# Kernel tuning notes

Hardware: AMD Instinct MI355X
Metric: run time of the kernel (lower is better)

## Reference

```python
import jax, jax.numpy as jnp
import numpy as np

HIDDEN = 768
HEADS = 12
HEAD_DIM = HIDDEN // HEADS

def setup_inputs() -> dict:
    key = jax.random.key(0)
    ks = jax.random.split(key, 9)
    s = 1.0 / np.sqrt(HIDDEN)
    x = jax.random.normal(ks[0], (2, 2048, HIDDEN), dtype=jnp.float32)
    Wq = jax.random.normal(ks[1], (HIDDEN, HIDDEN), dtype=jnp.float32) * s
    bq = jnp.zeros((HIDDEN,), dtype=jnp.float32)
    Wk = jax.random.normal(ks[2], (HIDDEN, HIDDEN), dtype=jnp.float32) * s
    bk = jnp.zeros((HIDDEN,), dtype=jnp.float32)
    Wv = jax.random.normal(ks[3], (HIDDEN, HIDDEN), dtype=jnp.float32) * s
    bv = jnp.zeros((HIDDEN,), dtype=jnp.float32)
    Wo = jax.random.normal(ks[4], (HIDDEN, HIDDEN), dtype=jnp.float32) * s
    bo = jnp.zeros((HIDDEN,), dtype=jnp.float32)
    return {"x": x, "Wq": Wq, "bq": bq, "Wk": Wk, "bk": bk,
            "Wv": Wv, "bv": bv, "Wo": Wo, "bo": bo}

def reference(x, Wq, bq, Wk, bk, Wv, bv, Wo, bo):
    B, S, _ = x.shape
    # project and split heads: [B, H, S, D]
    def proj(W, b):
        return (x @ W + b).reshape(B, S, HEADS, HEAD_DIM).transpose(0, 2, 1, 3)
    q = proj(Wq, bq)
    k = proj(Wk, bk)
    v = proj(Wv, bv)
    # NOTE: original module does NOT scale by 1/sqrt(head_dim)
    scores = jnp.einsum('bhqd,bhkd->bhqk', q, k)
    attn = jax.nn.softmax(scores, axis=-1)
    out = jnp.einsum('bhqk,bhkd->bhqd', attn, v)
    out = out.transpose(0, 2, 1, 3).reshape(B, S, HIDDEN)
    return out @ Wo + bo
```

## Files before the change

### kernel.cpp

```cpp
#include <hip/hip_runtime.h>
#include <cstddef>

#define HIDDEN 768
#define NHEADS 12
#define HDIM   64
#define BATCH  2
#define SEQ    2048
#define NROWS  (BATCH*SEQ)
#define LOG2E  1.4426950408889634f

typedef float f32x4  __attribute__((ext_vector_type(4)));
typedef float f32x16 __attribute__((ext_vector_type(16)));
typedef short bf16x8 __attribute__((ext_vector_type(8)));

__device__ __forceinline__ float fast_exp2(float x){
    return __builtin_amdgcn_exp2f(x);
}

__device__ __forceinline__ unsigned short f2bf(float f){
    unsigned u = __builtin_bit_cast(unsigned, f);
    u = u + 0x7FFFu + ((u >> 16) & 1u);
    return (unsigned short)(u >> 16);
}
__device__ __forceinline__ unsigned packbf2(float a, float b){
    unsigned ua = (__builtin_bit_cast(unsigned, a) + 0x8000u) >> 16;
    unsigned ub = (__builtin_bit_cast(unsigned, b) + 0x8000u) & 0xFFFF0000u;
    return ua | ub;
}
__device__ __forceinline__ unsigned cvtpk_bf16(float a, float b){
    unsigned r;
    asm("v_cvt_pk_bf16_f32 %0, %1, %2" : "=v"(r) : "v"(a), "v"(b));
    return r;
}

__device__ __forceinline__ void gl_lds16(const unsigned short* g, unsigned short* l){
    __builtin_amdgcn_global_load_lds(
        (const __attribute__((address_space(1))) unsigned int*)g,
        (__attribute__((address_space(3))) unsigned int*)l, 16, 0, 0);
}

__global__ __launch_bounds__(256) void cvt_bf16(const float* __restrict__ in,
                                                unsigned short* __restrict__ out,
                                                int n4)
{
    const int i = blockIdx.x * 256 + threadIdx.x;
    if (i >= n4) return;
    const float4 v = reinterpret_cast<const float4*>(in)[i];
    ushort4 o;
    o.x = f2bf(v.x); o.y = f2bf(v.y); o.z = f2bf(v.z); o.w = f2bf(v.w);
    reinterpret_cast<ushort4*>(out)[i] = o;
}

__global__ __launch_bounds__(256) void transpose_cvt4(const float* __restrict__ W0,
                                                      const float* __restrict__ W1,
                                                      const float* __restrict__ W2,
                                                      const float* __restrict__ W3,
                                                      unsigned short* __restrict__ T0,
                                                      unsigned short* __restrict__ T1,
                                                      unsigned short* __restrict__ T2,
                                                      unsigned short* __restrict__ T3)
{
    const int z = blockIdx.z;
    const float* W = (z == 0) ? W0 : (z == 1) ? W1 : (z == 2) ? W2 : W3;
    unsigned short* Wt = (z == 0) ? T0 : (z == 1) ? T1 : (z == 2) ? T2 : T3;

    __shared__ unsigned short t[64][66];
    const int k0 = blockIdx.y * 64, n0 = blockIdx.x * 64;
    const int row = threadIdx.x >> 2;
    const int c0  = (threadIdx.x & 3) * 16;
#pragma unroll
    for (int j = 0; j < 16; j += 4) {
        const float4 v = *reinterpret_cast<const float4*>(&W[(size_t)(k0 + row) * HIDDEN + n0 + c0 + j]);
        t[row][c0 + j + 0] = f2bf(v.x);
        t[row][c0 + j + 1] = f2bf(v.y);
        t[row][c0 + j + 2] = f2bf(v.z);
        t[row][c0 + j + 3] = f2bf(v.w);
    }
    __syncthreads();
#pragma unroll
    for (int j = 0; j < 16; j += 4) {
        ushort4 o;
        o.x = t[c0 + j + 0][row];
        o.y = t[c0 + j + 1][row];
        o.z = t[c0 + j + 2][row];
        o.w = t[c0 + j + 3][row];
        *reinterpret_cast<ushort4*>(&Wt[(size_t)(n0 + row) * HIDDEN + k0 + c0 + j]) = o;
    }
}

__device__ __forceinline__ void gemm_body(const unsigned short* __restrict__ A,
                                          const unsigned short* __restrict__ Wt,
                                          const float* __restrict__ bias,
                                          void* __restrict__ Cout, int mode,
                                          float scale,
                                          unsigned short* As, unsigned short* Bs)
{
    const int tid = threadIdx.x;
    const int l = tid & 63, w = tid >> 6;
    const int wm = w >> 1, wn = w & 1;
    const int l15 = l & 15, lg = l >> 4;
    const int srow = l >> 3, sslot = l & 7;
    const int m0 = blockIdx.y * 64, n0 = blockIdx.x * 96;

    f32x4 acc[2][3] = {};

    for (int k0 = 0; k0 < HIDDEN; k0 += 64) {
        __syncthreads();
#pragma unroll
        for (int a = 0; a < 2; ++a) {
            const int row = (a * 4 + w) * 8 + srow;
            const int sl = sslot ^ (row & 7);
            gl_lds16(&A[(size_t)(m0 + row) * HIDDEN + k0 + sl * 8], &As[(a * 4 + w) * 512]);
        }
#pragma unroll
        for (int b = 0; b < 3; ++b) {
            const int row = (b * 4 + w) * 8 + srow;
            const int sl = sslot ^ (row & 7);
            gl_lds16(&Wt[(size_t)(n0 + row) * HIDDEN + k0 + sl * 8], &Bs[(b * 4 + w) * 512]);
        }
        __syncthreads();

#pragma unroll
        for (int kk = 0; kk < 2; ++kk) {
            bf16x8 af[2], bfr[3];
#pragma unroll
            for (int mi = 0; mi < 2; ++mi) {
                const int r = wm * 32 + mi * 16 + l15;
                af[mi] = *reinterpret_cast<const bf16x8*>(&As[r * 64 + ((lg * 8 + kk * 32) ^ ((r & 7) << 3))]);
            }
#pragma unroll
            for (int ni = 0; ni < 3; ++ni) {
                const int r = wn * 48 + ni * 16 + l15;
                bfr[ni] = *reinterpret_cast<const bf16x8*>(&Bs[r * 64 + ((lg * 8 + kk * 32) ^ ((r & 7) << 3))]);
            }
#pragma unroll
            for (int mi = 0; mi < 2; ++mi)
#pragma unroll
                for (int ni = 0; ni < 3; ++ni)
                    acc[mi][ni] = __builtin_amdgcn_mfma_f32_16x16x32_bf16(af[mi], bfr[ni], acc[mi][ni], 0, 0, 0);
        }
    }

#pragma unroll
    for (int mi = 0; mi < 2; ++mi) {
#pragma unroll
        for (int ni = 0; ni < 3; ++ni) {
#pragma unroll
            for (int rr = 0; rr < 4; ++rr) {
                const int row = m0 + wm * 32 + mi * 16 + lg * 4 + rr;
                const int col = n0 + wn * 48 + ni * 16 + l15;
                const float v = (acc[mi][ni][rr] + bias[col]) * scale;
                if (mode == 0) {
                    const int b = row >> 11, s = row & (SEQ - 1);
                    const int hh = col >> 6, d = col & (HDIM - 1);
                    ((unsigned short*)Cout)[(((size_t)b * NHEADS + hh) * SEQ + s) * HDIM + d] = f2bf(v);
                } else if (mode == 1) {
                    const int b = row >> 11, s = row & (SEQ - 1);
                    const int hh = col >> 6, d = col & (HDIM - 1);
                    ((unsigned short*)Cout)[(((size_t)b * NHEADS + hh) * HDIM + d) * SEQ + s] = f2bf(v);
                } else {
                    ((float*)Cout)[(size_t)row * HIDDEN + col] = v;
                }
            }
        }
    }
}

__global__ __launch_bounds__(256) void qkv_gemm(const unsigned short* __restrict__ A,
                                                const unsigned short* __restrict__ Wqt,
                                                const unsigned short* __restrict__ Wkt,
                                                const unsigned short* __restrict__ Wvt,
                                                const float* __restrict__ bq,
                                                const float* __restrict__ bk,
                                                const float* __restrict__ bv,
                                                unsigned short* __restrict__ Qb,
                                                unsigned short* __restrict__ Kb,
                                                unsigned short* __restrict__ Vtb)
{
    __shared__ unsigned short As[64 * 64];
    __shared__ unsigned short Bs[96 * 64];
    const int z = blockIdx.z;
    const unsigned short* Wt = (z == 0) ? Wqt : (z == 1) ? Wkt : Wvt;
    const float* bias = (z == 0) ? bq : (z == 1) ? bk : bv;
    void* out = (z == 0) ? (void*)Qb : (z == 1) ? (void*)Kb : (void*)Vtb;
    const int mode = (z == 2) ? 1 : 0;
    const float scale = (z == 0) ? LOG2E : 1.0f;
    gemm_body(A, Wt, bias, out, mode, scale, As, Bs);
}

__global__ __launch_bounds__(256) void out_gemm(const unsigned short* __restrict__ A,
                                                const unsigned short* __restrict__ Wt,
                                                const float* __restrict__ bias,
                                                float* __restrict__ Cout)
{
    __shared__ unsigned short As[64 * 64];
    __shared__ unsigned short Bs[96 * 64];
    gemm_body(A, Wt, bias, Cout, 2, 1.0f, As, Bs);
}

__global__ __launch_bounds__(256, 4) void attn_mfma(const unsigned short* __restrict__ Q,
                                                    const unsigned short* __restrict__ K,
                                                    const unsigned short* __restrict__ Vt,
                                                    unsigned short* __restrict__ O)
{
    __shared__ __align__(16) char shraw[32768];
    unsigned short* shus = (unsigned short*)shraw;
    float*          pub  = (float*)shraw;
    float2*         mlx  = (float2*)(shraw + 24576);
    unsigned int*   Ep   = (unsigned int*)shraw;

    const int tid = threadIdx.x;
    const int l = tid & 63, w = tid >> 6;
    const int l31 = l & 31, hi = l >> 5;
    const int q0 = blockIdx.x * 32;
    const int h = blockIdx.y, b = blockIdx.z;
    const size_t base = ((size_t)b * NHEADS + h) * (size_t)SEQ * HDIM;

    unsigned short* Kb = shus + w * 4096;
    unsigned short* Vb = Kb + 2048;

    const int q = q0 + l31;
    bf16x8 qf[4];
#pragma unroll
    for (int t = 0; t < 4; ++t)
        qf[t] = *reinterpret_cast<const bf16x8*>(&Q[base + (size_t)q * HDIM + 16 * t + 8 * hi]);

    f32x16 accO[2] = {};
    float m = -1e30f, lsum = 0.f;

    const int klr = l >> 3, kslot = l & 7;
    const int vdl = l & 15, vjs = l >> 4;

    for (int t = 0; t < 16; ++t) {
        const int t0 = w * (SEQ / 4) + t * 32;

        asm volatile("s_waitcnt lgkmcnt(0)" ::: "memory");
#pragma unroll
        for (int c = 0; c < 4; ++c) {
            const int row = c * 8 + klr;
            const int sl = kslot ^ (row & 7);
            gl_lds16(&K[base + (size_t)(t0 + row) * HDIM + sl * 8], &Kb[c * 512]);
        }
#pragma unroll
        for (int c = 0; c < 4; ++c) {
            gl_lds16(&Vt[base + (size_t)(c * 16 + vdl) * SEQ + t0 + vjs * 8], &Vb[c * 512]);
        }
        asm volatile("s_waitcnt vmcnt(0)" ::: "memory");
        __builtin_amdgcn_sched_barrier(0);

        f32x16 sv = {};
        __builtin_amdgcn_s_setprio(1);
#pragma unroll
        for (int tt = 0; tt < 4; ++tt) {
            const int co = 16 * tt + 8 * hi;
            const bf16x8 kf = *reinterpret_cast<const bf16x8*>(&Kb[l31 * 64 + (co ^ ((l31 & 7) << 3))]);
            sv = __builtin_amdgcn_mfma_f32_32x32x16_bf16(kf, qf[tt], sv, 0, 0, 0);
        }
        __builtin_amdgcn_s_setprio(0);

        float tmax = -1e30f;
#pragma unroll
        for (int r = 0; r < 16; r += 4)
            tmax = fmaxf(tmax, fmaxf(fmaxf(sv[r], sv[r + 1]), fmaxf(sv[r + 2], sv[r + 3])));
        tmax = fmaxf(tmax, __shfl_xor(tmax, 32));

        if (tmax > m + 8.f) {
            const float scl = fast_exp2(m - tmax);
            lsum *= scl;
#pragma unroll
            for (int r = 0; r < 16; ++r) { accO[0][r] *= scl; accO[1][r] *= scl; }
            m = tmax;
        }

        unsigned wv[8];
        float ls = 0.f;
#pragma unroll
        for (int a = 0; a < 8; ++a) {
            const float pa = fast_exp2(sv[2 * a] - m);
            const float pb = fast_exp2(sv[2 * a + 1] - m);
            ls += pa + pb;
            wv[a] = cvtpk_bf16(pa, pb);
        }
        ls += __shfl_xor(ls, 32);
        lsum += ls;

#pragma unroll
        for (int s2 = 0; s2 < 2; ++s2) {
            const unsigned w0 = wv[s2 * 4 + 0], w1 = wv[s2 * 4 + 1];
            const unsigned w2 = wv[s2 * 4 + 2], w3 = wv[s2 * 4 + 3];
            const unsigned x0 = (unsigned)__shfl_xor((int)w0, 32);
            const unsigned x1 = (unsigned)__shfl_xor((int)w1, 32);
            const unsigned x2 = (unsigned)__shfl_xor((int)w2, 32);
            const unsigned x3 = (unsigned)__shfl_xor((int)w3, 32);
            uint4 fr;
            fr.x = hi ? x2 : w0;
            fr.y = hi ? x3 : w1;
            fr.z = hi ? w2 : x0;
            fr.w = hi ? w3 : x1;
            const bf16x8 pfrag = __builtin_bit_cast(bf16x8, fr);
            __builtin_amdgcn_s_setprio(1);
#pragma unroll
            for (int db = 0; db < 2; ++db) {
                const int d = 32 * db + l31;
                const int js = 2 * s2 + hi;
                const bf16x8 vf = *reinterpret_cast<const bf16x8*>(
                    &Vb[(d >> 4) * 512 + (js * 16 + (d & 15)) * 8]);
                accO[db] = __builtin_amdgcn_mfma_f32_32x32x16_bf16(vf, pfrag, accO[db], 0, 0, 0);
            }
            __builtin_amdgcn_s_setprio(0);
        }
    }

    __syncthreads();
    if (!hi) mlx[w * 32 + l31] = make_float2(m, lsum);
    __syncthreads();
    float M = -1e30f;
    float mj[4], lj[4];
#pragma unroll
    for (int j = 0; j < 4; ++j) {
        const float2 tml = mlx[j * 32 + l31];
        mj[j] = tml.x; lj[j] = tml.y;
        M = fmaxf(M, tml.x);
    }
    float lf = 0.f;
#pragma unroll
    for (int j = 0; j < 4; ++j) lf += lj[j] * fast_exp2(mj[j] - M);
    const float s = fast_exp2(m - M);
    const float inv = 1.f / lf;

    if (w != 0) {
#pragma unroll
        for (int db = 0; db < 2; ++db)
#pragma unroll
            for (int r = 0; r < 16; ++r) {
                const int d = 32 * db + (r & 3) + 8 * (r >> 2) + 4 * hi;
                pub[(w - 1) * 2048 + l31 * 64 + ((d + l31) & 63)] = accO[db][r] * s;
            }
    }
    __syncthreads();
    if (w == 0) {
#pragma unroll
        for (int db = 0; db < 2; ++db)
#pragma unroll
            for (int r = 0; r < 16; ++r) {
                const int d = 32 * db + (r & 3) + 8 * (r >> 2) + 4 * hi;
                float v = accO[db][r] * s;
#pragma unroll
                for (int wi = 0; wi < 3; ++wi)
                    v += pub[wi * 2048 + l31 * 64 + ((d + l31) & 63)];
                accO[db][r] = v * inv;
            }
        asm volatile("s_waitcnt lgkmcnt(0)" ::: "memory");
        __builtin_amdgcn_sched_barrier(0);
#pragma unroll
        for (int db = 0; db < 2; ++db)
#pragma unroll
            for (int a = 0; a < 8; ++a) {
                const unsigned wd = packbf2(accO[db][2 * a], accO[db][2 * a + 1]);
                const int pi = 16 * db + 4 * (a >> 1) + (a & 1) + 2 * hi;
                Ep[l31 * 33 + pi] = wd;
            }
        asm volatile("s_waitcnt lgkmcnt(0)" ::: "memory");
        __builtin_amdgcn_sched_barrier(0);
#pragma unroll
        for (int pss = 0; pss < 4; ++pss) {
            const int idx = pss * 64 + l;
            const int qr = idx >> 3, c = idx & 7;
            uint4 ov;
            ov.x = Ep[qr * 33 + c * 4 + 0];
            ov.y = Ep[qr * 33 + c * 4 + 1];
            ov.z = Ep[qr * 33 + c * 4 + 2];
            ov.w = Ep[qr * 33 + c * 4 + 3];
            *reinterpret_cast<uint4*>(&O[((size_t)b * SEQ + q0 + qr) * HIDDEN + h * HDIM + c * 8]) = ov;
        }
    }
}

extern "C" void kernel_launch(void* const* d_in, const int* in_sizes, int n_in,
                              void* d_out, int out_size, void* d_ws, size_t ws_size,
                              hipStream_t stream)
{
    const float* x  = (const float*)d_in[0];
    const float* Wq = (const float*)d_in[1];
    const float* bq = (const float*)d_in[2];
    const float* Wk = (const float*)d_in[3];
    const float* bk = (const float*)d_in[4];
    const float* Wv = (const float*)d_in[5];
    const float* bv = (const float*)d_in[6];
    const float* Wo = (const float*)d_in[7];
    const float* bo = (const float*)d_in[8];
    float* out = (float*)d_out;

    unsigned short* p = (unsigned short*)d_ws;
    const size_t szX = (size_t)NROWS * HIDDEN;
    const size_t szW = (size_t)HIDDEN * HIDDEN;
    const size_t szH = (size_t)BATCH * NHEADS * SEQ * HDIM;
    unsigned short* xb  = p;              p += szX;
    unsigned short* Wqt = p;              p += szW;
    unsigned short* Wkt = p;              p += szW;
    unsigned short* Wvt = p;              p += szW;
    unsigned short* Wot = p;              p += szW;
    unsigned short* Qb  = p;              p += szH;
    unsigned short* Kb  = p;              p += szH;
    unsigned short* Vtb = p;              p += szH;
    unsigned short* Oab = p;              p += szX;

    cvt_bf16<<<(int)(szX / 4 + 255) / 256, 256, 0, stream>>>(x, xb, (int)(szX / 4));
    transpose_cvt4<<<dim3(HIDDEN / 64, HIDDEN / 64, 4), 256, 0, stream>>>(
        Wq, Wk, Wv, Wo, Wqt, Wkt, Wvt, Wot);

    qkv_gemm<<<dim3(HIDDEN / 96, NROWS / 64, 3), 256, 0, stream>>>(
        xb, Wqt, Wkt, Wvt, bq, bk, bv, Qb, Kb, Vtb);

    attn_mfma<<<dim3(SEQ / 32, NHEADS, BATCH), 256, 0, stream>>>(Qb, Kb, Vtb, Oab);

    out_gemm<<<dim3(HIDDEN / 96, NROWS / 64), 256, 0, stream>>>(Oab, Wot, bo, out);
}
```

Measured before the change: 123.9 us.

## Double-buffer K/V loads in attention and split KV across two waves

The attention kernel drops from four waves per block to two, so each wave handles half of the key sequence. Each wave now double-buffers its K/V tiles in shared memory: it prefetches the next 32-key tile while computing on the current one, waiting with vmcnt(8) instead of fully draining. The cross-wave softmax merge is simplified to combine just two partial results. The intent is to hide global-load latency behind MFMA and softmax work, in exchange for longer serial per-wave loops, fewer waves per block, and the same 32KB of shared memory per block.

After: 139.5 us. 12.6% more time.

```diff
diff --git a/kernel.cpp b/kernel.cpp
--- a/kernel.cpp
+++ b/kernel.cpp
@@ -198,7 +198,7 @@
     gemm_body(A, Wt, bias, Cout, 2, 1.0f, As, Bs);
 }
 
-__global__ __launch_bounds__(256, 4) void attn_mfma(const unsigned short* __restrict__ Q,
+__global__ __launch_bounds__(128, 2) void attn_mfma(const unsigned short* __restrict__ Q,
                                                     const unsigned short* __restrict__ K,
                                                     const unsigned short* __restrict__ Vt,
                                                     unsigned short* __restrict__ O)
@@ -206,8 +206,8 @@
     __shared__ __align__(16) char shraw[32768];
     unsigned short* shus = (unsigned short*)shraw;
     float*          pub  = (float*)shraw;
-    float2*         mlx  = (float2*)(shraw + 24576);
-    unsigned int*   Ep   = (unsigned int*)shraw;
+    float2*         mlx  = (float2*)(shraw + 8192);
+    unsigned int*   Ep   = (unsigned int*)(shraw + 9216);
 
     const int tid = threadIdx.x;
     const int l = tid & 63, w = tid >> 6;
@@ -216,8 +216,7 @@
     const int h = blockIdx.y, b = blockIdx.z;
     const size_t base = ((size_t)b * NHEADS + h) * (size_t)SEQ * HDIM;
 
-    unsigned short* Kb = shus + w * 4096;
-    unsigned short* Vb = Kb + 2048;
+    unsigned short* Sb = shus + w * 8192;
 
     const int q = q0 + l31;
     bf16x8 qf[4];
@@ -230,111 +229,116 @@
 
     const int klr = l >> 3, kslot = l & 7;
     const int vdl = l & 15, vjs = l >> 4;
-
-    for (int t = 0; t < 16; ++t) {
-        const int t0 = w * (SEQ / 4) + t * 32;
-
-        asm volatile("s_waitcnt lgkmcnt(0)" ::: "memory");
-#pragma unroll
-        for (int c = 0; c < 4; ++c) {
-            const int row = c * 8 + klr;
-            const int sl = kslot ^ (row & 7);
-            gl_lds16(&K[base + (size_t)(t0 + row) * HDIM + sl * 8], &Kb[c * 512]);
-        }
-#pragma unroll
-        for (int c = 0; c < 4; ++c) {
-            gl_lds16(&Vt[base + (size_t)(c * 16 + vdl) * SEQ + t0 + vjs * 8], &Vb[c * 512]);
-        }
-        asm volatile("s_waitcnt vmcnt(0)" ::: "memory");
+    const int kvbase = w * (SEQ / 2);
+
+#define A_STAGE(buf, T0) do {                                                                 \
+    unsigned short* Kd = Sb + (buf) * 4096;                                                   \
+    unsigned short* Vd = Kd + 2048;                                                           \
+    _Pragma("unroll")                                                                         \
+    for (int c_ = 0; c_ < 4; ++c_) {                                                          \
+        const int row_ = c_ * 8 + klr;                                                        \
+        const int sl_ = kslot ^ (row_ & 7);                                                   \
+        gl_lds16(&K[base + (size_t)((T0) + row_) * HDIM + sl_ * 8], &Kd[c_ * 512]);           \
+    }                                                                                         \
+    _Pragma("unroll")                                                                         \
+    for (int c_ = 0; c_ < 4; ++c_) {                                                          \
+        gl_lds16(&Vt[base + (size_t)(c_ * 16 + vdl) * SEQ + (T0) + vjs * 8], &Vd[c_ * 512]);  \
+    }                                                                                         \
+    __builtin_amdgcn_sched_barrier(0);                                                        \
+} while (0)
+
+#define A_COMPUTE(buf) do {                                                                   \
+    unsigned short* Kb_ = Sb + (buf) * 4096;                                                  \
+    unsigned short* Vb_ = Kb_ + 2048;                                                         \
+    f32x16 sv = {};                                                                           \
+    __builtin_amdgcn_s_setprio(1);                                                            \
+    _Pragma("unroll")                                                                         \
+    for (int tt = 0; tt < 4; ++tt) {                                                          \
+        const int co = 16 * tt + 8 * hi;                                                      \
+        const bf16x8 kf = *reinterpret_cast<const bf16x8*>(&Kb_[l31 * 64 + (co ^ ((l31 & 7) << 3))]); \
+        sv = __builtin_amdgcn_mfma_f32_32x32x16_bf16(kf, qf[tt], sv, 0, 0, 0);                \
+    }                                                                                         \
+    __builtin_amdgcn_s_setprio(0);                                                            \
+    float tmax = -1e30f;                                                                      \
+    _Pragma("unroll")                                                                         \
+    for (int r_ = 0; r_ < 16; r_ += 4)                                                        \
+        tmax = fmaxf(tmax, fmaxf(fmaxf(sv[r_], sv[r_ + 1]), fmaxf(sv[r_ + 2], sv[r_ + 3])));  \
+    tmax = fmaxf(tmax, __shfl_xor(tmax, 32));                                                 \
+    if (tmax > m + 8.f) {                                                                     \
+        const float scl_ = fast_exp2(m - tmax);                                               \
+        lsum *= scl_;                                                                         \
+        _Pragma("unroll")                                                                     \
+        for (int r_ = 0; r_ < 16; ++r_) { accO[0][r_] *= scl_; accO[1][r_] *= scl_; }         \
+        m = tmax;                                                                             \
+    }                                                                                         \
+    unsigned wv[8];                                                                           \
+    float ls = 0.f;                                                                           \
+    _Pragma("unroll")                                                                         \
+    for (int a_ = 0; a_ < 8; ++a_) {                                                          \
+        const float pa_ = fast_exp2(sv[2 * a_] - m);                                          \
+        const float pb_ = fast_exp2(sv[2 * a_ + 1] - m);                                      \
+        ls += pa_ + pb_;                                                                      \
+        wv[a_] = cvtpk_bf16(pa_, pb_);                                                        \
+    }                                                                                         \
+    ls += __shfl_xor(ls, 32);                                                                 \
+    lsum += ls;                                                                               \
+    _Pragma("unroll")                                                                         \
+    for (int s2 = 0; s2 < 2; ++s2) {                                                          \
+        const unsigned w0 = wv[s2 * 4 + 0], w1 = wv[s2 * 4 + 1];                              \
+        const unsigned w2 = wv[s2 * 4 + 2], w3 = wv[s2 * 4 + 3];                              \
+        const unsigned x0 = (unsigned)__shfl_xor((int)w0, 32);                                \
+        const unsigned x1 = (unsigned)__shfl_xor((int)w1, 32);                                \
+        const unsigned x2 = (unsigned)__shfl_xor((int)w2, 32);                                \
+        const unsigned x3 = (unsigned)__shfl_xor((int)w3, 32);                                \
+        uint4 fr;                                                                             \
+        fr.x = hi ? x2 : w0;                                                                  \
+        fr.y = hi ? x3 : w1;                                                                  \
+        fr.z = hi ? w2 : x0;                                                                  \
+        fr.w = hi ? w3 : x1;                                                                  \
+        const bf16x8 pfrag = __builtin_bit_cast(bf16x8, fr);                                  \
+        __builtin_amdgcn_s_setprio(1);                                                        \
+        _Pragma("unroll")                                                                     \
+        for (int db = 0; db < 2; ++db) {                                                      \
+            const int d = 32 * db + l31;                                                      \
+            const int js = 2 * s2 + hi;                                                       \
+            const bf16x8 vf = *reinterpret_cast<const bf16x8*>(                               \
+                &Vb_[(d >> 4) * 512 + (js * 16 + (d & 15)) * 8]);                             \
+            accO[db] = __builtin_amdgcn_mfma_f32_32x32x16_bf16(vf, pfrag, accO[db], 0, 0, 0); \
+        }                                                                                     \
+        __builtin_amdgcn_s_setprio(0);                                                        \
+    }                                                                                         \
+} while (0)
+
+    A_STAGE(0, kvbase);
+#pragma unroll 2
+    for (int t = 0; t < 32; ++t) {
+        if (t + 1 < 32) {
+            asm volatile("s_waitcnt lgkmcnt(0)" ::: "memory");
+            A_STAGE((t + 1) & 1, kvbase + (t + 1) * 32);
+            asm volatile("s_waitcnt vmcnt(8)" ::: "memory");
+        } else {
+            asm volatile("s_waitcnt vmcnt(0)" ::: "memory");
+        }
         __builtin_amdgcn_sched_barrier(0);
-
-        f32x16 sv = {};
-        __builtin_amdgcn_s_setprio(1);
-#pragma unroll
-        for (int tt = 0; tt < 4; ++tt) {
-            const int co = 16 * tt + 8 * hi;
-            const bf16x8 kf = *reinterpret_cast<const bf16x8*>(&Kb[l31 * 64 + (co ^ ((l31 & 7) << 3))]);
-            sv = __builtin_amdgcn_mfma_f32_32x32x16_bf16(kf, qf[tt], sv, 0, 0, 0);
-        }
-        __builtin_amdgcn_s_setprio(0);
-
-        float tmax = -1e30f;
-#pragma unroll
-        for (int r = 0; r < 16; r += 4)
-            tmax = fmaxf(tmax, fmaxf(fmaxf(sv[r], sv[r + 1]), fmaxf(sv[r + 2], sv[r + 3])));
-        tmax = fmaxf(tmax, __shfl_xor(tmax, 32));
-
-        if (tmax > m + 8.f) {
-            const float scl = fast_exp2(m - tmax);
-            lsum *= scl;
-#pragma unroll
-            for (int r = 0; r < 16; ++r) { accO[0][r] *= scl; accO[1][r] *= scl; }
-            m = tmax;
-        }
-
-        unsigned wv[8];
-        float ls = 0.f;
-#pragma unroll
-        for (int a = 0; a < 8; ++a) {
-            const float pa = fast_exp2(sv[2 * a] - m);
-            const float pb = fast_exp2(sv[2 * a + 1] - m);
-            ls += pa + pb;
-            wv[a] = cvtpk_bf16(pa, pb);
-        }
-        ls += __shfl_xor(ls, 32);
-        lsum += ls;
-
-#pragma unroll
-        for (int s2 = 0; s2 < 2; ++s2) {
-            const unsigned w0 = wv[s2 * 4 + 0], w1 = wv[s2 * 4 + 1];
-            const unsigned w2 = wv[s2 * 4 + 2], w3 = wv[s2 * 4 + 3];
-            const unsigned x0 = (unsigned)__shfl_xor((int)w0, 32);
-            const unsigned x1 = (unsigned)__shfl_xor((int)w1, 32);
-            const unsigned x2 = (unsigned)__shfl_xor((int)w2, 32);
-            const unsigned x3 = (unsigned)__shfl_xor((int)w3, 32);
-            uint4 fr;
-            fr.x = hi ? x2 : w0;
-            fr.y = hi ? x3 : w1;
-            fr.z = hi ? w2 : x0;
-            fr.w = hi ? w3 : x1;
-            const bf16x8 pfrag = __builtin_bit_cast(bf16x8, fr);
-            __builtin_amdgcn_s_setprio(1);
-#pragma unroll
-            for (int db = 0; db < 2; ++db) {
-                const int d = 32 * db + l31;
-                const int js = 2 * s2 + hi;
-                const bf16x8 vf = *reinterpret_cast<const bf16x8*>(
-                    &Vb[(d >> 4) * 512 + (js * 16 + (d & 15)) * 8]);
-                accO[db] = __builtin_amdgcn_mfma_f32_32x32x16_bf16(vf, pfrag, accO[db], 0, 0, 0);
-            }
-            __builtin_amdgcn_s_setprio(0);
-        }
+        A_COMPUTE(t & 1);
     }
 
     __syncthreads();
     if (!hi) mlx[w * 32 + l31] = make_float2(m, lsum);
     __syncthreads();
-    float M = -1e30f;
-    float mj[4], lj[4];
-#pragma unroll
-    for (int j = 0; j < 4; ++j) {
-        const float2 tml = mlx[j * 32 + l31];
-        mj[j] = tml.x; lj[j] = tml.y;
-        M = fmaxf(M, tml.x);
-    }
-    float lf = 0.f;
-#pragma unroll
-    for (int j = 0; j < 4; ++j) lf += lj[j] * fast_exp2(mj[j] - M);
-    const float s = fast_exp2(m - M);
+    const float2 mp = mlx[(1 - w) * 32 + l31];
+    const float M  = fmaxf(m, mp.x);
+    const float s  = fast_exp2(m - M);
+    const float lf = lsum * s + mp.y * fast_exp2(mp.x - M);
     const float inv = 1.f / lf;
 
-    if (w != 0) {
+    if (w == 1) {
 #pragma unroll
         for (int db = 0; db < 2; ++db)
 #pragma unroll
             for (int r = 0; r < 16; ++r) {
                 const int d = 32 * db + (r & 3) + 8 * (r >> 2) + 4 * hi;
-                pub[(w - 1) * 2048 + l31 * 64 + ((d + l31) & 63)] = accO[db][r] * s;
+                pub[l31 * 64 + ((d + l31) & 63)] = accO[db][r] * s;
             }
     }
     __syncthreads();
@@ -344,11 +348,7 @@
 #pragma unroll
             for (int r = 0; r < 16; ++r) {
                 const int d = 32 * db + (r & 3) + 8 * (r >> 2) + 4 * hi;
-                float v = accO[db][r] * s;
-#pragma unroll
-                for (int wi = 0; wi < 3; ++wi)
-                    v += pub[wi * 2048 + l31 * 64 + ((d + l31) & 63)];
-                accO[db][r] = v * inv;
+                accO[db][r] = (accO[db][r] * s + pub[l31 * 64 + ((d + l31) & 63)]) * inv;
             }
         asm volatile("s_waitcnt lgkmcnt(0)" ::: "memory");
         __builtin_amdgcn_sched_barrier(0);
@@ -374,6 +374,8 @@
             *reinterpret_cast<uint4*>(&O[((size_t)b * SEQ + q0 + qr) * HIDDEN + h * HDIM + c * 8]) = ov;
         }
     }
+#undef A_STAGE
+#undef A_COMPUTE
 }
 
 extern "C" void kernel_launch(void* const* d_in, const int* in_sizes, int n_in,
@@ -412,7 +414,7 @@
     qkv_gemm<<<dim3(HIDDEN / 96, NROWS / 64, 3), 256, 0, stream>>>(
         xb, Wqt, Wkt, Wvt, bq, bk, bv, Qb, Kb, Vtb);
 
-    attn_mfma<<<dim3(SEQ / 32, NHEADS, BATCH), 256, 0, stream>>>(Qb, Kb, Vtb, Oab);
+    attn_mfma<<<dim3(SEQ / 32, NHEADS, BATCH), 128, 0, stream>>>(Qb, Kb, Vtb, Oab);
 
     out_gemm<<<dim3(HIDDEN / 96, NROWS / 64), 256, 0, stream>>>(Oab, Wot, bo, out);
 }
```
